# Optimization experiments

Hardware: AMD Instinct MI355X
Metric: run time of the kernel (lower is better)

Reference implementation:

```python
import jax, jax.numpy as jnp
import numpy as np
import math

# ---------- real Wigner 3j tensors (e3nn real basis convention), built once ----------

def _su2_cg(j1, m1, j2, m2, j3, m3):
    if m3 != m1 + m2:
        return 0.0
    f = math.factorial
    vmin = max(-j1 + j2 + m3, -j1 + m1, 0)
    vmax = min(j2 + j3 + m1, j3 - j1 + j2, j3 + m3)
    c = ((2 * j3 + 1) * f(j3 + j1 - j2) * f(j3 - j1 + j2) * f(j1 + j2 - j3) / f(j1 + j2 + j3 + 1)) ** 0.5
    c *= (f(j3 + m3) * f(j3 - m3) * f(j1 - m1) * f(j1 + m1) * f(j2 - m2) * f(j2 + m2)) ** 0.5
    s = 0.0
    for v in range(vmin, vmax + 1):
        s += (-1.0) ** (v + j2 + m2) * f(j2 + j3 + m1 - v) * f(j1 - m1 + v) / (
            f(v) * f(j3 - j1 + j2 - v) * f(j3 + m3 - v) * f(v + j1 - j2 - m3))
    return c * s

def _q(l):
    # real -> complex change of basis (e3nn convention)
    q = np.zeros((2 * l + 1, 2 * l + 1), dtype=np.complex128)
    for m in range(-l, 0):
        q[l + m, l + abs(m)] = 1 / np.sqrt(2)
        q[l + m, l - abs(m)] = -1j / np.sqrt(2)
    q[l, l] = 1.0
    for m in range(1, l + 1):
        q[l + m, l + abs(m)] = (-1) ** m / np.sqrt(2)
        q[l + m, l - abs(m)] = 1j * ((-1) ** m) / np.sqrt(2)
    return ((-1j) ** l) * q

def _w3j(l1, l2, l3):
    c = np.zeros((2 * l1 + 1, 2 * l2 + 1, 2 * l3 + 1))
    for m1 in range(-l1, l1 + 1):
        for m2 in range(-l2, l2 + 1):
            m3 = m1 + m2
            if abs(m3) <= l3:
                c[l1 + m1, l2 + m2, l3 + m3] = _su2_cg(l1, m1, l2, m2, l3, m3)
    cr = np.einsum('ij,kl,nm,ikn->jlm', _q(l1), _q(l2), np.conj(_q(l3)), c.astype(np.complex128))
    cr = np.real(cr)
    return (cr / np.linalg.norm(cr)).astype(np.float32)  # unit Frobenius norm, like e3nn

C444 = jnp.asarray(_w3j(4, 4, 4)); C464 = jnp.asarray(_w3j(4, 6, 4))
C644 = jnp.asarray(_w3j(6, 4, 4)); C664 = jnp.asarray(_w3j(6, 6, 4))
C446 = jnp.asarray(_w3j(4, 4, 6)); C466 = jnp.asarray(_w3j(4, 6, 6))
C646 = jnp.asarray(_w3j(6, 4, 6)); C666 = jnp.asarray(_w3j(6, 6, 6))
C424 = jnp.asarray(_w3j(4, 2, 4)); C624 = jnp.asarray(_w3j(6, 2, 4))
C426 = jnp.asarray(_w3j(4, 2, 6)); C626 = jnp.asarray(_w3j(6, 2, 6))

def _sh_kernel():
    # spherical harmonics 1x0e + 1x2e (integral normalization) at the 4 fixed kernel dirs
    s = 1.0 / np.sqrt(2.0)
    dirs = np.array([[-s, -s, 0.0], [s, -s, 0.0], [-s, s, 0.0], [s, s, 0.0]])
    x, y, z = dirs[:, 0], dirs[:, 1], dirs[:, 2]
    y0 = np.full(4, 0.5 / np.sqrt(np.pi))
    k = 0.5 * np.sqrt(15.0 / np.pi)
    y2 = np.stack([k * x * y, k * y * z, 0.25 * np.sqrt(5.0 / np.pi) * (3 * z * z - 1.0),
                   k * z * x, 0.5 * k * (x * x - y * y)], -1)
    return jnp.asarray(np.concatenate([y0[:, None], y2], -1).astype(np.float32))  # (4, 6)

SH = _sh_kernel()

# ---------- FullyConnectedTensorProduct kernels (mult=1 per irrep -> scalar path weights) ----------

def _tp_ff(x1, x2, w):
    # (1x4e+1x6e) x (1x4e+1x6e) -> (1x4e+1x6e); 8 CG-allowed paths.
    # path_weight = sqrt(dim_out / n_paths_into_out): sqrt(9/4)=1.5, sqrt(13/4)=sqrt(13)/2
    a4, a6 = x1[:, :9], x1[:, 9:]
    b4, b6 = x2[:, :9], x2[:, 9:]
    E = lambda a, b, c: jnp.einsum('ni,nj,ijk->nk', a, b, c)
    out4 = 1.5 * (w[0] * E(a4, b4, C444) + w[1] * E(a4, b6, C464)
                  + w[2] * E(a6, b4, C644) + w[3] * E(a6, b6, C664))
    out6 = (math.sqrt(13.0) / 2.0) * (w[4] * E(a4, b4, C446) + w[5] * E(a4, b6, C466)
                  + w[6] * E(a6, b4, C646) + w[7] * E(a6, b6, C666))
    return jnp.concatenate([out4, out6], -1)

def _tp_fsh(p, w):
    # (1x4e+1x6e) x (1x0e+1x2e) -> (1x4e+1x6e), summed over the 4 neighbours.
    # 6 paths; 3 into each output -> path_weight sqrt(9/3), sqrt(13/3).
    a4, a6 = p[:, :, :9], p[:, :, 9:]  # (N,4,9), (N,4,13)
    sh0, sh2 = SH[:, 0], SH[:, 1:]
    Ep = lambda a, c: jnp.einsum('npi,pj,ijk->nk', a, sh2, c)
    E0 = lambda a: jnp.einsum('npi,p->ni', a, sh0)
    # w3j(l,0,l) = identity / sqrt(2l+1)
    out4 = math.sqrt(3.0) * (w[0] * E0(a4) / 3.0 + w[1] * Ep(a4, C424) + w[2] * Ep(a6, C624))
    out6 = math.sqrt(13.0 / 3.0) * (w[3] * Ep(a4, C426) + w[4] * E0(a6) / math.sqrt(13.0)
                                    + w[5] * Ep(a6, C626))
    return jnp.concatenate([out4, out6], -1)

def _forward(f4, f6, H, W, spatial_weights, w_sp, w_agg, w_tp):
    R, C = 4, 22
    feats = jnp.concatenate([f4, f6], -1).reshape(H, W, C)
    # ---- EquivariantSpatialConv (kernel 3, replicate pad, residual) ----
    fp = jnp.pad(feats, ((1, 1), (1, 1), (0, 0)), mode='edge')
    neigh = jnp.zeros_like(feats)
    for di in range(3):
        for dj in range(3):
            neigh = neigh + spatial_weights[di, dj] * fp[di:di + H, dj:dj + W]
    x = feats.reshape(-1, C)
    x = x + _tp_ff(x, neigh.reshape(-1, C), w_sp)
    # ---- EquivariantUpsampleConv (nearest x4, SH-aggregated 2x2 context, residual) ----
    img = x.reshape(H, W, C)
    hr = jnp.repeat(jnp.repeat(img, R, axis=0), R, axis=1)  # (Hr, Wr, C)
    Hr, Wr = H * R, W * R
    hp = jnp.pad(hr, ((0, 1), (0, 1), (0, 0)), mode='edge')
    # unfold(2,2,1).unfold(3,2,1) -> 4 neighbours in row-major (0,0),(0,1),(1,0),(1,1) order
    p = jnp.stack([hp[:Hr, :Wr], hp[:Hr, 1:Wr + 1], hp[1:Hr + 1, :Wr], hp[1:Hr + 1, 1:Wr + 1]],
                  axis=2).reshape(-1, 4, C)
    context = _tp_fsh(p, w_agg)  # (N, C)
    ff = hr.reshape(-1, C)
    out = _tp_ff(ff, context, w_tp)
    return out[:, :9] + ff[:, :9], out[:, 9:] + ff[:, 9:]

def setup_inputs() -> dict:
    key = jax.random.key(0)
    k0, k1, k2, k3, k4, k5 = jax.random.split(key, 6)
    H = W = 128
    N = H * W
    f4 = jax.random.normal(k0, (N, 9), dtype=jnp.float32)
    f6 = jax.random.normal(k1, (N, 13), dtype=jnp.float32)
    spatial_weights = jnp.full((3, 3), 1.0 / 9.0, dtype=jnp.float32) \
        + 0.05 * jax.random.uniform(k2, (3, 3), dtype=jnp.float32)
    w_sp = 0.3 * jax.random.normal(k3, (8,), dtype=jnp.float32)
    w_agg = 0.3 * jax.random.normal(k4, (6,), dtype=jnp.float32)
    w_tp = 0.3 * jax.random.normal(k5, (8,), dtype=jnp.float32)
    return {'f4': f4, 'f6': f6, 'H': H, 'W': W, 'spatial_weights': spatial_weights,
            'w_sp': w_sp, 'w_agg': w_agg, 'w_tp': w_tp}

def reference(f4, f6, H, W, spatial_weights, w_sp, w_agg, w_tp):
    return _forward(f4, f6, H, W, spatial_weights, w_sp, w_agg, w_tp)
```

## Files before the change

kernel.cpp:

```cpp
#include <hip/hip_runtime.h>

#define DEV __device__ __forceinline__

#define OFF444 0
#define OFF464 729
#define OFF644 1782
#define OFF664 2835
#define OFF446 4356
#define OFF466 5409
#define OFF646 6930
#define OFF666 8451
#define OFF424 10648
#define OFF624 11053
#define OFF426 11638
#define OFF626 12223
#define NC_TOT 13068

__device__ float gC[NC_TOT];
__device__ float gSH[24];
__device__ float gX[16384 * 22];

__device__ const int gL1t[12] = {4,4,6,6,4,4,6,6,4,6,4,6};
__device__ const int gL2t[12] = {4,6,4,6,4,6,4,6,2,2,2,2};
__device__ const int gL3t[12] = {4,4,4,4,6,6,6,6,4,4,6,6};
__device__ const int gOFFt[12]= {OFF444,OFF464,OFF644,OFF664,OFF446,OFF466,OFF646,OFF666,
                                 OFF424,OFF624,OFF426,OFF626};

DEV double dfact(int n){ double r = 1.0; for(int i = 2; i <= n; ++i) r *= (double)i; return r; }

DEV double su2_cg(const double* F, int j1,int m1,int j2,int m2,int j3,int m3){
  if(m1 + m2 != m3) return 0.0;
  int vmin = -j1 + j2 + m3;
  if(-j1 + m1 > vmin) vmin = -j1 + m1;
  if(0 > vmin) vmin = 0;
  int vmax = j2 + j3 + m1;
  if(j3 - j1 + j2 < vmax) vmax = j3 - j1 + j2;
  if(j3 + m3 < vmax) vmax = j3 + m3;
  if(vmax < vmin) return 0.0;
  double c = sqrt((2.0*j3 + 1.0) * F[j3+j1-j2] * F[j3-j1+j2] * F[j1+j2-j3] / F[j1+j2+j3+1]);
  c *= sqrt(F[j3+m3]*F[j3-m3]*F[j1-m1]*F[j1+m1]*F[j2-m2]*F[j2+m2]);
  double s = 0.0;
  for(int v = vmin; v <= vmax; ++v){
    double term = F[j2+j3+m1-v]*F[j1-m1+v] /
                  (F[v]*F[j3-j1+j2-v]*F[j3+m3-v]*F[v+j1-j2-m3]);
    s += ((v + j2 + m2) & 1) ? -term : term;
  }
  return c * s;
}

DEV void qentry(int l, int i, int j, double& outr, double& outi){
  const double s = 0.70710678118654752440;
  int m = i - l;
  double ar = 0.0, ai = 0.0;
  if(m < 0){
    if(j == l - m) ar = s;
    else if(j == l + m) ai = -s;
  } else if(m == 0){
    if(j == l) ar = 1.0;
  } else {
    double sg = (m & 1) ? -1.0 : 1.0;
    if(j == l + m) ar = sg * s;
    else if(j == l - m) ai = sg * s;
  }
  int lm = l & 3;
  if(lm == 0){ outr = ar;  outi = ai;  }
  else if(lm == 1){ outr = ai;  outi = -ar; }
  else if(lm == 2){ outr = -ar; outi = -ai; }
  else { outr = -ai; outi = ar; }
}

__global__ __launch_bounds__(256) void init_w3j(){
  __shared__ double F[24];
  __shared__ double red[256];
  __shared__ double s_scale;
  const int tid = threadIdx.x;
  if(tid < 24) F[tid] = dfact(tid);
  __syncthreads();
  const int b  = blockIdx.x;
  if(b == 0 && tid == 0){
    const double PI = 3.14159265358979323846;
    const double sv = 0.70710678118654752440;
    double dx[4] = {-sv, sv, -sv, sv};
    double dy[4] = {-sv, -sv, sv, sv};
    double kk = 0.5 * sqrt(15.0 / PI);
    for(int p = 0; p < 4; ++p){
      double x = dx[p], y = dy[p], z = 0.0;
      gSH[p*6+0] = (float)(0.5 / sqrt(PI));
      gSH[p*6+1] = (float)(kk * x * y);
      gSH[p*6+2] = (float)(kk * y * z);
      gSH[p*6+3] = (float)(0.25 * sqrt(5.0 / PI) * (3.0*z*z - 1.0));
      gSH[p*6+4] = (float)(kk * z * x);
      gSH[p*6+5] = (float)(0.5 * kk * (x*x - y*y));
    }
  }
  const int l1 = gL1t[b], l2 = gL2t[b], l3 = gL3t[b];
  const int d2 = 2*l2 + 1, d3 = 2*l3 + 1;
  const int total = (2*l1+1) * d2 * d3;
  const int off = gOFFt[b];
  double ss = 0.0;
  for(int t = tid; t < total; t += 256){
    int mo = t % d3; int r = t / d3; int lo = r % d2; int jo = r / d2;
    int ci[2]; int ni = 1; ci[0] = jo; if(jo != 2*l1 - jo){ ci[1] = 2*l1 - jo; ni = 2; }
    int ck[2]; int nk = 1; ck[0] = lo; if(lo != 2*l2 - lo){ ck[1] = 2*l2 - lo; nk = 2; }
    int cn[2]; int nn = 1; cn[0] = mo; if(mo != 2*l3 - mo){ cn[1] = 2*l3 - mo; nn = 2; }
    double acc = 0.0;
    for(int a = 0; a < ni; ++a){
      int i = ci[a];
      double q1r, q1i; qentry(l1, i, jo, q1r, q1i);
      if(q1r == 0.0 && q1i == 0.0) continue;
      for(int bq = 0; bq < nk; ++bq){
        int k = ck[bq];
        double q2r, q2i; qentry(l2, k, lo, q2r, q2i);
        if(q2r == 0.0 && q2i == 0.0) continue;
        double r12 = q1r*q2r - q1i*q2i;
        double i12 = q1r*q2i + q1i*q2r;
        for(int cq = 0; cq < nn; ++cq){
          int n = cn[cq];
          double q3r, q3i; qentry(l3, n, mo, q3r, q3i);
          if(q3r == 0.0 && q3i == 0.0) continue;
          double cg = su2_cg(F, l1, i-l1, l2, k-l2, l3, n-l3);
          if(cg == 0.0) continue;
          acc += (r12*q3r + i12*q3i) * cg;
        }
      }
    }
    gC[off + t] = (float)acc;
    ss += acc * acc;
  }
  red[tid] = ss;
  __syncthreads();
  for(int stp = 128; stp > 0; stp >>= 1){
    if(tid < stp) red[tid] += red[tid + stp];
    __syncthreads();
  }
  if(tid == 0) s_scale = 1.0 / sqrt(red[0]);
  __syncthreads();
  float sc = (float)s_scale;
  for(int t = tid; t < total; t += 256) gC[off + t] *= sc;
}

DEV void tp_ff_core(const float* __restrict__ sC,
                    const float* __restrict__ pa4, const float* __restrict__ pa6,
                    const float* b4, const float* b6, const float* sw,
                    float* o4, float* o6){
  #pragma unroll 1
  for(int i = 0; i < 9; ++i){
    float ai = pa4[i];
    const float* __restrict__ c444 = sC + OFF444 + i*81;
    const float* __restrict__ c446 = sC + OFF446 + i*117;
    const float* __restrict__ c464 = sC + OFF464 + i*117;
    const float* __restrict__ c466 = sC + OFF466 + i*169;
    #pragma unroll
    for(int j = 0; j < 9; ++j){
      float t = ai * b4[j]; float t4 = t * sw[0]; float t6 = t * sw[4];
      #pragma unroll
      for(int k = 0; k < 9; ++k)  o4[k] = fmaf(c444[j*9 + k],  t4, o4[k]);
      #pragma unroll
      for(int k = 0; k < 13; ++k) o6[k] = fmaf(c446[j*13 + k], t6, o6[k]);
    }
    #pragma unroll
    for(int j = 0; j < 13; ++j){
      float t = ai * b6[j]; float t4 = t * sw[1]; float t6 = t * sw[5];
      #pragma unroll
      for(int k = 0; k < 9; ++k)  o4[k] = fmaf(c464[j*9 + k],  t4, o4[k]);
      #pragma unroll
      for(int k = 0; k < 13; ++k) o6[k] = fmaf(c466[j*13 + k], t6, o6[k]);
    }
  }
  #pragma unroll 1
  for(int i = 0; i < 13; ++i){
    float ai = pa6[i];
    const float* __restrict__ c644 = sC + OFF644 + i*81;
    const float* __restrict__ c646 = sC + OFF646 + i*117;
    const float* __restrict__ c664 = sC + OFF664 + i*117;
    const float* __restrict__ c666 = sC + OFF666 + i*169;
    #pragma unroll
    for(int j = 0; j < 9; ++j){
      float t = ai * b4[j]; float t4 = t * sw[2]; float t6 = t * sw[6];
      #pragma unroll
      for(int k = 0; k < 9; ++k)  o4[k] = fmaf(c644[j*9 + k],  t4, o4[k]);
      #pragma unroll
      for(int k = 0; k < 13; ++k) o6[k] = fmaf(c646[j*13 + k], t6, o6[k]);
    }
    #pragma unroll
    for(int j = 0; j < 13; ++j){
      float t = ai * b6[j]; float t4 = t * sw[3]; float t6 = t * sw[7];
      #pragma unroll
      for(int k = 0; k < 9; ++k)  o4[k] = fmaf(c664[j*9 + k],  t4, o4[k]);
      #pragma unroll
      for(int k = 0; k < 13; ++k) o6[k] = fmaf(c666[j*13 + k], t6, o6[k]);
    }
  }
}

__global__ __launch_bounds__(256) void stage_a(
    const float* __restrict__ f4, const float* __restrict__ f6,
    const int* __restrict__ pH, const int* __restrict__ pW,
    const float* __restrict__ spw, const float* __restrict__ wsp,
    float* __restrict__ xws, int useg, int N){
  __shared__ float sC[NC_TOT];
  for(int t = threadIdx.x; t < NC_TOT; t += 256) sC[t] = gC[t];
  __syncthreads();
  int n = blockIdx.x * 256 + threadIdx.x;
  if(n >= N) return;
  int H = *pH, W = *pW;
  int i = n / W, j = n - i * W;
  float nb[22];
  #pragma unroll
  for(int c = 0; c < 22; ++c) nb[c] = 0.f;
  #pragma unroll
  for(int di = 0; di < 3; ++di){
    int ip = i + di - 1; ip = ip < 0 ? 0 : (ip >= H ? H - 1 : ip);
    #pragma unroll
    for(int dj = 0; dj < 3; ++dj){
      int jp = j + dj - 1; jp = jp < 0 ? 0 : (jp >= W ? W - 1 : jp);
      float wg = spw[di*3 + dj];
      const float* q4 = f4 + (ip * W + jp) * 9;
      const float* q6 = f6 + (ip * W + jp) * 13;
      #pragma unroll
      for(int c = 0; c < 9; ++c)  nb[c]     = fmaf(wg, q4[c], nb[c]);
      #pragma unroll
      for(int c = 0; c < 13; ++c) nb[9 + c] = fmaf(wg, q6[c], nb[9 + c]);
    }
  }
  float sw[8];
  #pragma unroll
  for(int t = 0; t < 4; ++t) sw[t] = 1.5f * wsp[t];
  #pragma unroll
  for(int t = 4; t < 8; ++t) sw[t] = 1.80277563773199465f * wsp[t];
  float o4[9], o6[13];
  #pragma unroll
  for(int k = 0; k < 9; ++k)  o4[k] = 0.f;
  #pragma unroll
  for(int k = 0; k < 13; ++k) o6[k] = 0.f;
  tp_ff_core(sC, f4 + n*9, f6 + n*13, nb, nb + 9, sw, o4, o6);
  float* xo = (useg ? gX : xws) + n * 22;
  #pragma unroll
  for(int k = 0; k < 9; ++k)  xo[k]     = f4[n*9 + k]  + o4[k];
  #pragma unroll
  for(int k = 0; k < 13; ++k) xo[9 + k] = f6[n*13 + k] + o6[k];
}

__global__ __launch_bounds__(256) void stage_b(
    const float* __restrict__ xws, int useg,
    const int* __restrict__ pH, const int* __restrict__ pW,
    const float* __restrict__ wagg, const float* __restrict__ wtp,
    float* __restrict__ out, int N){
  __shared__ float sC[NC_TOT];
  for(int t = threadIdx.x; t < NC_TOT; t += 256) sC[t] = gC[t];
  __syncthreads();
  int n2 = blockIdx.x * 256 + threadIdx.x;
  if(n2 >= 4*N) return;
  const float* __restrict__ x = useg ? gX : xws;
  int H = *pH, W = *pW;
  int Wr = W * 4;
  int cell = n2 >> 2, v = n2 & 3;
  int il = cell / W, jl = cell - il * W;
  int bi = v >> 1, bj = v & 1;
  int il2 = bi ? (il + 1 < H ? il + 1 : H - 1) : il;
  int jl2 = bj ? (jl + 1 < W ? jl + 1 : W - 1) : jl;
  const float* __restrict__ p0 = x + (il  * W + jl ) * 22;
  const float* __restrict__ p1 = x + (il  * W + jl2) * 22;
  const float* __restrict__ p2 = x + (il2 * W + jl ) * 22;
  const float* __restrict__ p3 = x + (il2 * W + jl2) * 22;

  const float SQ3   = 1.73205080756887729f;
  const float SQ133 = 2.08166599946613263f;
  const float RS13  = 0.27735009811261457f;

  float sh0v[4], sh2v[4][5];
  #pragma unroll
  for(int p = 0; p < 4; ++p){
    sh0v[p] = gSH[p*6];
    #pragma unroll
    for(int j = 0; j < 5; ++j) sh2v[p][j] = gSH[p*6 + 1 + j];
  }
  float w0 = wagg[0], w1 = wagg[1], w2 = wagg[2], w3 = wagg[3], w4 = wagg[4], w5 = wagg[5];
  float c4e0 = SQ3 * (1.0f/3.0f) * w0;
  float c6e0 = SQ133 * RS13 * w4;
  float c41 = SQ3 * w1,   c42 = SQ3 * w2;
  float c63 = SQ133 * w3, c65 = SQ133 * w5;

  float ctx4[9], ctx6[13];
  #pragma unroll
  for(int k = 0; k < 9; ++k)  ctx4[k] = 0.f;
  #pragma unroll
  for(int k = 0; k < 13; ++k) ctx6[k] = 0.f;

  #pragma unroll 1
  for(int i = 0; i < 9; ++i){
    float a0 = p0[i], a1 = p1[i], a2 = p2[i], a3 = p3[i];
    float m0 = a0*sh0v[0] + a1*sh0v[1] + a2*sh0v[2] + a3*sh0v[3];
    ctx4[i] += c4e0 * m0;
    #pragma unroll
    for(int j = 0; j < 5; ++j){
      float m = a0*sh2v[0][j] + a1*sh2v[1][j] + a2*sh2v[2][j] + a3*sh2v[3][j];
      float f1 = c41 * m, f3 = c63 * m;
      const float* __restrict__ cA = sC + OFF424 + (i*5 + j)*9;
      const float* __restrict__ cB = sC + OFF426 + (i*5 + j)*13;
      #pragma unroll
      for(int k = 0; k < 9; ++k)  ctx4[k] = fmaf(f1, cA[k], ctx4[k]);
      #pragma unroll
      for(int k = 0; k < 13; ++k) ctx6[k] = fmaf(f3, cB[k], ctx6[k]);
    }
  }
  #pragma unroll 1
  for(int i = 0; i < 13; ++i){
    float a0 = p0[9+i], a1 = p1[9+i], a2 = p2[9+i], a3 = p3[9+i];
    float m0 = a0*sh0v[0] + a1*sh0v[1] + a2*sh0v[2] + a3*sh0v[3];
    ctx6[i] += c6e0 * m0;
    #pragma unroll
    for(int j = 0; j < 5; ++j){
      float m = a0*sh2v[0][j] + a1*sh2v[1][j] + a2*sh2v[2][j] + a3*sh2v[3][j];
      float f2 = c42 * m, f5 = c65 * m;
      const float* __restrict__ cA = sC + OFF624 + (i*5 + j)*9;
      const float* __restrict__ cB = sC + OFF626 + (i*5 + j)*13;
      #pragma unroll
      for(int k = 0; k < 9; ++k)  ctx4[k] = fmaf(f2, cA[k], ctx4[k]);
      #pragma unroll
      for(int k = 0; k < 13; ++k) ctx6[k] = fmaf(f5, cB[k], ctx6[k]);
    }
  }

  float sw[8];
  #pragma unroll
  for(int t = 0; t < 4; ++t) sw[t] = 1.5f * wtp[t];
  #pragma unroll
  for(int t = 4; t < 8; ++t) sw[t] = 1.80277563773199465f * wtp[t];
  float o4[9], o6[13];
  #pragma unroll
  for(int k = 0; k < 9; ++k)  o4[k] = 0.f;
  #pragma unroll
  for(int k = 0; k < 13; ++k) o6[k] = 0.f;
  tp_ff_core(sC, p0, p0 + 9, ctx4, ctx6, sw, o4, o6);

  float r4[9], r6[13];
  #pragma unroll
  for(int k = 0; k < 9; ++k)  r4[k] = o4[k] + p0[k];
  #pragma unroll
  for(int k = 0; k < 13; ++k) r6[k] = o6[k] + p0[9 + k];

  size_t Nr = (size_t)N * 16;
  int r0 = bi ? 3 : 0, rcnt = bi ? 1 : 3;
  int c0 = bj ? 3 : 0, ccnt = bj ? 1 : 3;
  for(int dr = 0; dr < rcnt; ++dr){
    int ir = il*4 + r0 + dr;
    for(int dc = 0; dc < ccnt; ++dc){
      int jr = jl*4 + c0 + dc;
      size_t np = (size_t)ir * Wr + jr;
      float* out4 = out + np * 9;
      float* out6 = out + Nr * 9 + np * 13;
      #pragma unroll
      for(int k = 0; k < 9; ++k)  out4[k] = r4[k];
      #pragma unroll
      for(int k = 0; k < 13; ++k) out6[k] = r6[k];
    }
  }
}

extern "C" void kernel_launch(void* const* d_in, const int* in_sizes, int n_in,
                              void* d_out, int out_size, void* d_ws, size_t ws_size,
                              hipStream_t stream){
  const float* f4   = (const float*)d_in[0];
  const float* f6   = (const float*)d_in[1];
  const int*   pH   = (const int*)d_in[2];
  const int*   pW   = (const int*)d_in[3];
  const float* spw  = (const float*)d_in[4];
  const float* wsp  = (const float*)d_in[5];
  const float* wagg = (const float*)d_in[6];
  const float* wtp  = (const float*)d_in[7];
  int N  = in_sizes[0] / 9;
  int useg = (N <= 16384) ? 1 : 0;
  float* x = (float*)d_ws;

  hipLaunchKernelGGL(init_w3j, dim3(12), dim3(256), 0, stream);
  hipLaunchKernelGGL(stage_a, dim3((N + 255)/256), dim3(256), 0, stream,
                     f4, f6, pH, pW, spw, wsp, x, useg, N);
  hipLaunchKernelGGL(stage_b, dim3((4*N + 255)/256), dim3(256), 0, stream,
                     x, useg, pH, pW, wagg, wtp, (float*)d_out, N);
}
```

Baseline: 347.1 us.

## Split per-point tensor-product work across four lanes with shuffle reduction

Each point in stage_a and each subcell in stage_b is now handled by four threads. Each thread takes a strided share of the 22 input components and accumulates partial outputs, which are then summed with xor shuffles; output writes are also split across the lanes. The init kernel moves to 1024 threads per block and the shared-memory coefficient copy uses float4 loads. This adds parallelism and shortens each thread's serial FMA chain, at the cost of redundant neighborhood loads per lane, extra shuffles, and 4x more blocks that each reload the coefficient table into shared memory.

```diff
diff --git a/kernel.cpp b/kernel.cpp
--- a/kernel.cpp
+++ b/kernel.cpp
@@ -16,7 +16,7 @@
 #define OFF626 12223
 #define NC_TOT 13068
 
-__device__ float gC[NC_TOT];
+__device__ __align__(16) float gC[NC_TOT];
 __device__ float gSH[24];
 __device__ float gX[16384 * 22];
 
@@ -69,9 +69,9 @@
   else { outr = -ai; outi = ar; }
 }
 
-__global__ __launch_bounds__(256) void init_w3j(){
+__global__ __launch_bounds__(1024) void init_w3j(){
   __shared__ double F[24];
-  __shared__ double red[256];
+  __shared__ double red[1024];
   __shared__ double s_scale;
   const int tid = threadIdx.x;
   if(tid < 24) F[tid] = dfact(tid);
@@ -98,7 +98,7 @@
   const int total = (2*l1+1) * d2 * d3;
   const int off = gOFFt[b];
   double ss = 0.0;
-  for(int t = tid; t < total; t += 256){
+  for(int t = tid; t < total; t += 1024){
     int mo = t % d3; int r = t / d3; int lo = r % d2; int jo = r / d2;
     int ci[2]; int ni = 1; ci[0] = jo; if(jo != 2*l1 - jo){ ci[1] = 2*l1 - jo; ni = 2; }
     int ck[2]; int nk = 1; ck[0] = lo; if(lo != 2*l2 - lo){ ck[1] = 2*l2 - lo; nk = 2; }
@@ -129,67 +129,58 @@
   }
   red[tid] = ss;
   __syncthreads();
-  for(int stp = 128; stp > 0; stp >>= 1){
+  for(int stp = 512; stp > 0; stp >>= 1){
     if(tid < stp) red[tid] += red[tid + stp];
     __syncthreads();
   }
   if(tid == 0) s_scale = 1.0 / sqrt(red[0]);
   __syncthreads();
   float sc = (float)s_scale;
-  for(int t = tid; t < total; t += 256) gC[off + t] *= sc;
-}
-
-DEV void tp_ff_core(const float* __restrict__ sC,
-                    const float* __restrict__ pa4, const float* __restrict__ pa6,
-                    const float* b4, const float* b6, const float* sw,
-                    float* o4, float* o6){
-  #pragma unroll 1
-  for(int i = 0; i < 9; ++i){
-    float ai = pa4[i];
-    const float* __restrict__ c444 = sC + OFF444 + i*81;
-    const float* __restrict__ c446 = sC + OFF446 + i*117;
-    const float* __restrict__ c464 = sC + OFF464 + i*117;
-    const float* __restrict__ c466 = sC + OFF466 + i*169;
+  for(int t = tid; t < total; t += 1024) gC[off + t] *= sc;
+}
+
+DEV void tp_quad(const float* __restrict__ sC, int lane,
+                 const float* __restrict__ a4, const float* __restrict__ a6,
+                 const float* b4, const float* b6, const float* sw,
+                 float* o4, float* o6){
+  for(int ii = lane; ii < 22; ii += 4){
+    const bool is4 = ii < 9;
+    const int il = is4 ? ii : ii - 9;
+    const float ai = is4 ? a4[il] : a6[il];
+    const float* __restrict__ cA4 = sC + (is4 ? OFF444 + il*81  : OFF644 + il*81);
+    const float* __restrict__ cA6 = sC + (is4 ? OFF446 + il*117 : OFF646 + il*117);
+    const float* __restrict__ cB4 = sC + (is4 ? OFF464 + il*117 : OFF664 + il*117);
+    const float* __restrict__ cB6 = sC + (is4 ? OFF466 + il*169 : OFF666 + il*169);
+    const float s4a = is4 ? sw[0] : sw[2];
+    const float s6a = is4 ? sw[4] : sw[6];
+    const float s4b = is4 ? sw[1] : sw[3];
+    const float s6b = is4 ? sw[5] : sw[7];
     #pragma unroll
     for(int j = 0; j < 9; ++j){
-      float t = ai * b4[j]; float t4 = t * sw[0]; float t6 = t * sw[4];
-      #pragma unroll
-      for(int k = 0; k < 9; ++k)  o4[k] = fmaf(c444[j*9 + k],  t4, o4[k]);
-      #pragma unroll
-      for(int k = 0; k < 13; ++k) o6[k] = fmaf(c446[j*13 + k], t6, o6[k]);
+      float t = ai * b4[j]; float t4 = t * s4a, t6 = t * s6a;
+      #pragma unroll
+      for(int k = 0; k < 9; ++k)  o4[k] = fmaf(cA4[j*9 + k],  t4, o4[k]);
+      #pragma unroll
+      for(int k = 0; k < 13; ++k) o6[k] = fmaf(cA6[j*13 + k], t6, o6[k]);
     }
     #pragma unroll
     for(int j = 0; j < 13; ++j){
-      float t = ai * b6[j]; float t4 = t * sw[1]; float t6 = t * sw[5];
-      #pragma unroll
-      for(int k = 0; k < 9; ++k)  o4[k] = fmaf(c464[j*9 + k],  t4, o4[k]);
-      #pragma unroll
-      for(int k = 0; k < 13; ++k) o6[k] = fmaf(c466[j*13 + k], t6, o6[k]);
-    }
-  }
-  #pragma unroll 1
-  for(int i = 0; i < 13; ++i){
-    float ai = pa6[i];
-    const float* __restrict__ c644 = sC + OFF644 + i*81;
-    const float* __restrict__ c646 = sC + OFF646 + i*117;
-    const float* __restrict__ c664 = sC + OFF664 + i*117;
-    const float* __restrict__ c666 = sC + OFF666 + i*169;
-    #pragma unroll
-    for(int j = 0; j < 9; ++j){
-      float t = ai * b4[j]; float t4 = t * sw[2]; float t6 = t * sw[6];
-      #pragma unroll
-      for(int k = 0; k < 9; ++k)  o4[k] = fmaf(c644[j*9 + k],  t4, o4[k]);
-      #pragma unroll
-      for(int k = 0; k < 13; ++k) o6[k] = fmaf(c646[j*13 + k], t6, o6[k]);
-    }
-    #pragma unroll
-    for(int j = 0; j < 13; ++j){
-      float t = ai * b6[j]; float t4 = t * sw[3]; float t6 = t * sw[7];
-      #pragma unroll
-      for(int k = 0; k < 9; ++k)  o4[k] = fmaf(c664[j*9 + k],  t4, o4[k]);
-      #pragma unroll
-      for(int k = 0; k < 13; ++k) o6[k] = fmaf(c666[j*13 + k], t6, o6[k]);
-    }
+      float t = ai * b6[j]; float t4 = t * s4b, t6 = t * s6b;
+      #pragma unroll
+      for(int k = 0; k < 9; ++k)  o4[k] = fmaf(cB4[j*9 + k],  t4, o4[k]);
+      #pragma unroll
+      for(int k = 0; k < 13; ++k) o6[k] = fmaf(cB6[j*13 + k], t6, o6[k]);
+    }
+  }
+  #pragma unroll
+  for(int k = 0; k < 9; ++k){
+    o4[k] += __shfl_xor(o4[k], 1);
+    o4[k] += __shfl_xor(o4[k], 2);
+  }
+  #pragma unroll
+  for(int k = 0; k < 13; ++k){
+    o6[k] += __shfl_xor(o6[k], 1);
+    o6[k] += __shfl_xor(o6[k], 2);
   }
 }
 
@@ -198,10 +189,15 @@
     const int* __restrict__ pH, const int* __restrict__ pW,
     const float* __restrict__ spw, const float* __restrict__ wsp,
     float* __restrict__ xws, int useg, int N){
-  __shared__ float sC[NC_TOT];
-  for(int t = threadIdx.x; t < NC_TOT; t += 256) sC[t] = gC[t];
-  __syncthreads();
-  int n = blockIdx.x * 256 + threadIdx.x;
+  __shared__ __align__(16) float sC[NC_TOT];
+  {
+    float4* s4p = (float4*)sC;
+    const float4* g4p = (const float4*)gC;
+    for(int t = threadIdx.x; t < NC_TOT/4; t += 256) s4p[t] = g4p[t];
+  }
+  __syncthreads();
+  int gid = blockIdx.x * 256 + threadIdx.x;
+  int n = gid >> 2, lane = gid & 3;
   if(n >= N) return;
   int H = *pH, W = *pW;
   int i = n / W, j = n - i * W;
@@ -233,12 +229,10 @@
   for(int k = 0; k < 9; ++k)  o4[k] = 0.f;
   #pragma unroll
   for(int k = 0; k < 13; ++k) o6[k] = 0.f;
-  tp_ff_core(sC, f4 + n*9, f6 + n*13, nb, nb + 9, sw, o4, o6);
+  tp_quad(sC, lane, f4 + n*9, f6 + n*13, nb, nb + 9, sw, o4, o6);
   float* xo = (useg ? gX : xws) + n * 22;
-  #pragma unroll
-  for(int k = 0; k < 9; ++k)  xo[k]     = f4[n*9 + k]  + o4[k];
-  #pragma unroll
-  for(int k = 0; k < 13; ++k) xo[9 + k] = f6[n*13 + k] + o6[k];
+  for(int k = lane; k < 9; k += 4)  xo[k]     = f4[n*9 + k]  + o4[k];
+  for(int k = lane; k < 13; k += 4) xo[9 + k] = f6[n*13 + k] + o6[k];
 }
 
 __global__ __launch_bounds__(256) void stage_b(
@@ -246,15 +240,20 @@
     const int* __restrict__ pH, const int* __restrict__ pW,
     const float* __restrict__ wagg, const float* __restrict__ wtp,
     float* __restrict__ out, int N){
-  __shared__ float sC[NC_TOT];
-  for(int t = threadIdx.x; t < NC_TOT; t += 256) sC[t] = gC[t];
-  __syncthreads();
-  int n2 = blockIdx.x * 256 + threadIdx.x;
-  if(n2 >= 4*N) return;
+  __shared__ __align__(16) float sC[NC_TOT];
+  {
+    float4* s4p = (float4*)sC;
+    const float4* g4p = (const float4*)gC;
+    for(int t = threadIdx.x; t < NC_TOT/4; t += 256) s4p[t] = g4p[t];
+  }
+  __syncthreads();
+  int gid = blockIdx.x * 256 + threadIdx.x;
+  int t2 = gid >> 2, lane = gid & 3;
+  if(t2 >= 4*N) return;
   const float* __restrict__ x = useg ? gX : xws;
   int H = *pH, W = *pW;
   int Wr = W * 4;
-  int cell = n2 >> 2, v = n2 & 3;
+  int cell = t2 >> 2, v = t2 & 3;
   int il = cell / W, jl = cell - il * W;
   int bi = v >> 1, bj = v & 1;
   int il2 = bi ? (il + 1 < H ? il + 1 : H - 1) : il;
@@ -286,40 +285,35 @@
   for(int k = 0; k < 9; ++k)  ctx4[k] = 0.f;
   #pragma unroll
   for(int k = 0; k < 13; ++k) ctx6[k] = 0.f;
-
-  #pragma unroll 1
-  for(int i = 0; i < 9; ++i){
-    float a0 = p0[i], a1 = p1[i], a2 = p2[i], a3 = p3[i];
+  for(int ii = lane; ii < 22; ii += 4){
+    const bool is4 = ii < 9;
+    const int ilr = is4 ? ii : ii - 9;
+    float a0 = p0[ii], a1 = p1[ii], a2 = p2[ii], a3 = p3[ii];
     float m0 = a0*sh0v[0] + a1*sh0v[1] + a2*sh0v[2] + a3*sh0v[3];
-    ctx4[i] += c4e0 * m0;
+    if(is4) ctx4[ilr] += c4e0 * m0; else ctx6[ilr] += c6e0 * m0;
+    const float* __restrict__ cA = sC + (is4 ? OFF424 + ilr*45 : OFF624 + ilr*45);
+    const float* __restrict__ cB = sC + (is4 ? OFF426 + ilr*65 : OFF626 + ilr*65);
+    const float fA = is4 ? c41 : c42;
+    const float fB = is4 ? c63 : c65;
     #pragma unroll
     for(int j = 0; j < 5; ++j){
       float m = a0*sh2v[0][j] + a1*sh2v[1][j] + a2*sh2v[2][j] + a3*sh2v[3][j];
-      float f1 = c41 * m, f3 = c63 * m;
-      const float* __restrict__ cA = sC + OFF424 + (i*5 + j)*9;
-      const float* __restrict__ cB = sC + OFF426 + (i*5 + j)*13;
-      #pragma unroll
-      for(int k = 0; k < 9; ++k)  ctx4[k] = fmaf(f1, cA[k], ctx4[k]);
-      #pragma unroll
-      for(int k = 0; k < 13; ++k) ctx6[k] = fmaf(f3, cB[k], ctx6[k]);
-    }
-  }
-  #pragma unroll 1
-  for(int i = 0; i < 13; ++i){
-    float a0 = p0[9+i], a1 = p1[9+i], a2 = p2[9+i], a3 = p3[9+i];
-    float m0 = a0*sh0v[0] + a1*sh0v[1] + a2*sh0v[2] + a3*sh0v[3];
-    ctx6[i] += c6e0 * m0;
-    #pragma unroll
-    for(int j = 0; j < 5; ++j){
-      float m = a0*sh2v[0][j] + a1*sh2v[1][j] + a2*sh2v[2][j] + a3*sh2v[3][j];
-      float f2 = c42 * m, f5 = c65 * m;
-      const float* __restrict__ cA = sC + OFF624 + (i*5 + j)*9;
-      const float* __restrict__ cB = sC + OFF626 + (i*5 + j)*13;
-      #pragma unroll
-      for(int k = 0; k < 9; ++k)  ctx4[k] = fmaf(f2, cA[k], ctx4[k]);
-      #pragma unroll
-      for(int k = 0; k < 13; ++k) ctx6[k] = fmaf(f5, cB[k], ctx6[k]);
-    }
+      float f1 = fA * m, f3 = fB * m;
+      #pragma unroll
+      for(int k = 0; k < 9; ++k)  ctx4[k] = fmaf(f1, cA[j*9 + k], ctx4[k]);
+      #pragma unroll
+      for(int k = 0; k < 13; ++k) ctx6[k] = fmaf(f3, cB[j*13 + k], ctx6[k]);
+    }
+  }
+  #pragma unroll
+  for(int k = 0; k < 9; ++k){
+    ctx4[k] += __shfl_xor(ctx4[k], 1);
+    ctx4[k] += __shfl_xor(ctx4[k], 2);
+  }
+  #pragma unroll
+  for(int k = 0; k < 13; ++k){
+    ctx6[k] += __shfl_xor(ctx6[k], 1);
+    ctx6[k] += __shfl_xor(ctx6[k], 2);
   }
 
   float sw[8];
@@ -332,13 +326,7 @@
   for(int k = 0; k < 9; ++k)  o4[k] = 0.f;
   #pragma unroll
   for(int k = 0; k < 13; ++k) o6[k] = 0.f;
-  tp_ff_core(sC, p0, p0 + 9, ctx4, ctx6, sw, o4, o6);
-
-  float r4[9], r6[13];
-  #pragma unroll
-  for(int k = 0; k < 9; ++k)  r4[k] = o4[k] + p0[k];
-  #pragma unroll
-  for(int k = 0; k < 13; ++k) r6[k] = o6[k] + p0[9 + k];
+  tp_quad(sC, lane, p0, p0 + 9, ctx4, ctx6, sw, o4, o6);
 
   size_t Nr = (size_t)N * 16;
   int r0 = bi ? 3 : 0, rcnt = bi ? 1 : 3;
@@ -350,10 +338,8 @@
       size_t np = (size_t)ir * Wr + jr;
       float* out4 = out + np * 9;
       float* out6 = out + Nr * 9 + np * 13;
-      #pragma unroll
-      for(int k = 0; k < 9; ++k)  out4[k] = r4[k];
-      #pragma unroll
-      for(int k = 0; k < 13; ++k) out6[k] = r6[k];
+      for(int k = lane; k < 9; k += 4)  out4[k] = o4[k] + p0[k];
+      for(int k = lane; k < 13; k += 4) out6[k] = o6[k] + p0[9 + k];
     }
   }
 }
@@ -373,9 +359,9 @@
   int useg = (N <= 16384) ? 1 : 0;
   float* x = (float*)d_ws;
 
-  hipLaunchKernelGGL(init_w3j, dim3(12), dim3(256), 0, stream);
-  hipLaunchKernelGGL(stage_a, dim3((N + 255)/256), dim3(256), 0, stream,
+  hipLaunchKernelGGL(init_w3j, dim3(12), dim3(1024), 0, stream);
+  hipLaunchKernelGGL(stage_a, dim3((4*N + 255)/256), dim3(256), 0, stream,
                      f4, f6, pH, pW, spw, wsp, x, useg, N);
-  hipLaunchKernelGGL(stage_b, dim3((4*N + 255)/256), dim3(256), 0, stream,
+  hipLaunchKernelGGL(stage_b, dim3((16*N + 255)/256), dim3(256), 0, stream,
                      x, useg, pH, pW, wagg, wtp, (float*)d_out, N);
 }
```

Measured after the change: 280.1 us. 1.24x faster.
